# Kernel tuning notes

Hardware: AMD Instinct MI355X
Metric: run time of the kernel (lower is better)

The kernel has to match this reference:

```python
import jax, jax.numpy as jnp
import numpy as np
from jax import lax

H, P, N, G, K, CHUNK = 64, 64, 128, 1, 4, 256
D_MODEL = 2048
D_INNER = H * P            # 4096
CONV_DIM = D_INNER + 2 * G * N  # 4352
EPS = 1e-5


def setup_inputs() -> dict:
    key = jax.random.key(0)
    ks = jax.random.split(key, 6)
    s = lambda k, shape, scale: jax.random.normal(k, shape, jnp.float32) * scale
    return {
        "hidden_states": s(ks[0], (2, 2048, D_MODEL), 1.0),
        "in_proj_w": s(ks[1], (D_MODEL, D_INNER + CONV_DIM + H), D_MODEL ** -0.5),
        "conv_w": s(ks[2], (CONV_DIM, K), K ** -0.5),
        "conv_b": jnp.zeros((CONV_DIM,), jnp.float32),
        "dt_bias": jnp.ones((H,), jnp.float32),
        "A_log": jnp.log(jnp.arange(1, H + 1, dtype=jnp.float32)),
        "D_param": jnp.ones((H,), jnp.float32),
        "norm_w": jnp.ones((D_INNER,), jnp.float32),
        "out_proj_w": s(ks[3], (D_INNER, D_MODEL), D_INNER ** -0.5),
    }


def _mamba2_forward(hidden_states, in_proj_w, conv_w, conv_b, dt_bias, A_log, D_param, norm_w, out_proj_w):
    b, l, _ = hidden_states.shape
    c = l // CHUNK  # number of chunks

    # in_proj -> gate | conv channels (x,B,C) | dt
    proj = hidden_states @ in_proj_w
    gate = proj[..., :D_INNER]
    hbc = proj[..., D_INNER:D_INNER + CONV_DIM]
    dt = proj[..., D_INNER + CONV_DIM:]  # [b,l,H]

    # depthwise causal conv1d + silu
    xt = hbc.transpose(0, 2, 1)  # [b, CONV_DIM, l]
    y = lax.conv_general_dilated(
        xt, conv_w[:, None, :], window_strides=(1,), padding=[(K - 1, 0)],
        feature_group_count=CONV_DIM, dimension_numbers=("NCH", "OIH", "NCH"))
    hbc = jax.nn.silu(y + conv_b[None, :, None]).transpose(0, 2, 1)  # [b,l,CONV_DIM]

    # split into x / B / C per group (unflatten over groups as in torch code)
    per_g = D_INNER // G
    hg = hbc.reshape(b, l, G, per_g + 2 * N)
    x = hg[..., :per_g].reshape(b, l, H, P)                 # [b,l,h,p]
    Bm = hg[..., per_g:per_g + N]                            # [b,l,g,n]
    Cm = hg[..., per_g + N:]                                 # [b,l,g,n]
    hpg = H // G
    Bh = jnp.repeat(Bm, hpg, axis=2)                         # [b,l,h,n]
    Ch = jnp.repeat(Cm, hpg, axis=2)

    # dt: softplus(dt + bias), clamp per time_step_limit (0, inf)
    dt = jax.nn.softplus(dt + dt_bias)                       # [b,l,h]
    A = -jnp.exp(A_log)                                      # [h]

    # chunk the sequence
    x_c = x.reshape(b, c, CHUNK, H, P)
    B_c = Bh.reshape(b, c, CHUNK, H, N)
    C_c = Ch.reshape(b, c, CHUNK, H, N)
    dt_c = dt.reshape(b, c, CHUNK, H)

    dA = dt_c * A[None, None, None, :]                       # [b,c,L,h]
    cum = jnp.cumsum(dA, axis=2)                             # [b,c,L,h]

    # intra-chunk (diagonal block): decay[i,j] = exp(cum_i - cum_j), i>=j
    diff = cum[:, :, :, None, :] - cum[:, :, None, :, :]     # [b,c,i,j,h]
    i = jnp.arange(CHUNK)
    mask = i[:, None] >= i[None, :]
    decay = jnp.exp(jnp.where(mask[None, None, :, :, None], diff, -jnp.inf))
    scores = jnp.einsum("bcihn,bcjhn->bcijh", C_c, B_c) * decay * dt_c[:, :, None, :, :]
    Y_diag = jnp.einsum("bcijh,bcjhp->bcihp", scores, x_c)   # [b,c,L,h,p]

    # per-chunk final states
    decay_states = jnp.exp(cum[:, :, -1:, :] - cum)          # [b,c,L,h]
    states = jnp.einsum("bclh,bclhn,bclhp->bchpn", decay_states * dt_c, B_c, x_c)
    chunk_decay = jnp.exp(cum[:, :, -1, :])                  # [b,c,h]

    # inter-chunk recurrence over chunks
    def step(prev, inp):
        st, cd = inp  # [b,h,p,n], [b,h]
        new = cd[:, :, None, None] * prev + st
        return new, prev

    init = jnp.zeros((b, H, P, N), hidden_states.dtype)
    _, prev_states = lax.scan(step, init, (jnp.moveaxis(states, 1, 0), jnp.moveaxis(chunk_decay, 1, 0)))
    prev_states = jnp.moveaxis(prev_states, 0, 1)            # [b,c,h,p,n]

    state_decay_out = jnp.exp(cum)                           # [b,c,L,h]
    Y_off = jnp.einsum("bclhn,bchpn,bclh->bclhp", C_c, prev_states, state_decay_out)

    yh = (Y_diag + Y_off).reshape(b, l, H, P) + D_param[None, None, :, None] * x
    yr = yh.reshape(b, l, D_INNER)

    # gated RMSNorm
    hidden = yr * jax.nn.silu(gate)
    var = jnp.mean(hidden * hidden, axis=-1, keepdims=True)
    hidden = hidden * lax.rsqrt(var + EPS) * norm_w

    return hidden @ out_proj_w


def reference(hidden_states, in_proj_w, conv_w, conv_b, dt_bias, A_log, D_param, norm_w, out_proj_w):
    return _mamba2_forward(hidden_states, in_proj_w, conv_w, conv_b, dt_bias, A_log, D_param, norm_w, out_proj_w)
```

## Files before the change

kernel.cpp:

```cpp
#include <hip/hip_runtime.h>
#include <hip/hip_bf16.h>


typedef __attribute__((ext_vector_type(8))) _Float16 f16x8;
typedef __attribute__((ext_vector_type(4))) float f32x4;

#define GLD16(gp, lp) __builtin_amdgcn_global_load_lds( \
    (__attribute__((address_space(1))) void*)(gp),      \
    (__attribute__((address_space(3))) void*)(lp), 16, 0, 0)

__device__ __forceinline__ unsigned short f2h(float v) {
  _Float16 h = (_Float16)v;
  return *reinterpret_cast<unsigned short*>(&h);
}
__device__ __forceinline__ float h2f(unsigned short u) {
  _Float16 h = *reinterpret_cast<_Float16*>(&u);
  return (float)h;
}
__device__ __forceinline__ float siluf(float x) { return x / (1.f + expf(-x)); }

__global__ __launch_bounds__(256) void prep(const float* __restrict__ hs,
                                            const float* __restrict__ Win,
                                            _Float16* __restrict__ Ah,
                                            _Float16* __restrict__ WtH,
                                            float* __restrict__ zf) {
  __shared__ __attribute__((aligned(16))) char smemP[32768];
  const int bid = blockIdx.x;
  const int tid = threadIdx.x;
  if (bid < 1024) {
    float (*Xs)[2048] = reinterpret_cast<float (*)[2048]>(smemP);
    int t0 = bid * 4;
#pragma unroll
    for (int i = 0; i < 8; i++) {
      int e = tid * 4 + i * 1024;
      int tok = e >> 11, k = e & 2047;
      *reinterpret_cast<float4*>(&Xs[tok][k]) =
          *reinterpret_cast<const float4*>(&hs[(long)(t0 + tok) * 2048 + k]);
    }
    __syncthreads();
    int h = tid & 63, tg = tid >> 6;
    float a0 = 0.f, a1 = 0.f, a2 = 0.f, a3 = 0.f;
    const float* wcol = Win + 8448 + h;
    for (int k = 0; k < 2048; k += 4) {
      a0 = fmaf(Xs[tg][k + 0], wcol[(long)(k + 0) * 8512], a0);
      a1 = fmaf(Xs[tg][k + 1], wcol[(long)(k + 1) * 8512], a1);
      a2 = fmaf(Xs[tg][k + 2], wcol[(long)(k + 2) * 8512], a2);
      a3 = fmaf(Xs[tg][k + 3], wcol[(long)(k + 3) * 8512], a3);
    }
    zf[(long)(t0 + tg) * 64 + h] = (a0 + a1) + (a2 + a3);
  } else if (bid < 9216) {
    long i = ((long)(bid - 1024) * 256 + tid) * 4;
    float4 v = *reinterpret_cast<const float4*>(hs + i);
    ushort4 u;
    u.x = f2h(v.x); u.y = f2h(v.y); u.z = f2h(v.z); u.w = f2h(v.w);
    *reinterpret_cast<ushort4*>((unsigned short*)Ah + i) = u;
  } else {
    float (*tile)[33] = reinterpret_cast<float (*)[33]>(smemP);
    int i = bid - 9216;
    int c0 = (i % 264) * 32, r0 = (i / 264) * 32;
    int tx = tid & 31, ty = tid >> 5;
#pragma unroll
    for (int j = 0; j < 4; j++)
      tile[ty + j * 8][tx] = Win[(long)(r0 + ty + j * 8) * 8512 + c0 + tx];
    __syncthreads();
#pragma unroll
    for (int j = 0; j < 4; j++) {
      int c = c0 + ty + j * 8, r = r0 + tx;
      WtH[(long)c * 2048 + r] = (_Float16)tile[tx][ty + j * 8];
    }
  }
}

__global__ __launch_bounds__(512, 2) void gemm_in8(const _Float16* __restrict__ A,
                                                   const _Float16* __restrict__ Bt,
                                                   _Float16* __restrict__ gate,
                                                   float* __restrict__ hbcf,
                                                   float* __restrict__ rparts) {
  __shared__ __attribute__((aligned(128))) char ldsB[131072];
  const int tid = threadIdx.x;
  const int lane = tid & 63;
  const int wv = tid >> 6;
  const int wr = wv >> 2, wc = wv & 3;
  const int wg = blockIdx.x;
  const bool rem = wg >= 512;
  int by, bxn, kbase, zz;
  if (!rem) {
    const int xcd = wg & 7, j = wg >> 3;
    by = (xcd >> 2) * 8 + (j >> 3);
    bxn = (xcd & 3) * 8 + (j & 7);
    kbase = 0; zz = 0;
  } else {
    const int idx = wg - 512;
    by = idx & 15; zz = idx >> 4; bxn = 32; kbase = zz * 256;
  }

  const int srow = tid >> 3;
  const int scolg = (tid & 7) ^ (srow & 7);
  const _Float16* Ab = A + (long)by * 524288 + (long)srow * 2048 + scolg * 8 + kbase;
  const _Float16* Bb = Bt + (long)bxn * 524288 + (long)srow * 2048 + scolg * 8 + kbase;
  const int ldst = tid << 4;

#define STAGE_A(tau, h) do {                                              \
    const _Float16* g_ = Ab + (long)(h) * 262144 + (tau) * 64;            \
    char* l_ = ldsB + ((((tau) & 1) << 2) + (h)) * 16384 + ldst;          \
    GLD16(g_, l_); GLD16(g_ + 131072, l_ + 8192); } while (0)
#define STAGE_B(tau, h) do {                                              \
    const _Float16* g_ = Bb + (long)(h) * 262144 + (tau) * 64;            \
    char* l_ = ldsB + ((((tau) & 1) << 2) + 2 + (h)) * 16384 + ldst;      \
    GLD16(g_, l_); GLD16(g_ + 131072, l_ + 8192); } while (0)

  const int fr = lane & 15;
  const int c16 = (lane >> 4) ^ (fr & 7);
  const int aOff0 = wr * 16384 + fr * 128 + c16 * 16;
  const int aOff1 = aOff0 ^ 64;
  const int bOff0 = (2 + (wc >> 1)) * 16384 + ((wc & 1) * 64 + fr) * 128 + c16 * 16;
  const int bOff1 = bOff0 ^ 64;
#define RD_A(b, mi, k32) (*(const f16x8*)(ldsB + ((k32) ? aOff1 : aOff0) + (b) * 65536 + (mi) * 2048))
#define RD_B(b, ni, k32) (*(const f16x8*)(ldsB + ((k32) ? bOff1 : bOff0) + (b) * 65536 + (ni) * 2048))

#define BAR() __builtin_amdgcn_s_barrier()
#define WLG0() asm volatile("s_waitcnt lgkmcnt(0)" ::: "memory")
#define WLG8() asm volatile("s_waitcnt lgkmcnt(8)" ::: "memory")
#define WVM4() asm volatile("s_waitcnt vmcnt(4)" ::: "memory")

  f32x4 acc[8][4];
#pragma unroll
  for (int mi = 0; mi < 8; ++mi)
#pragma unroll
    for (int ni = 0; ni < 4; ++ni) acc[mi][ni] = f32x4{0.f, 0.f, 0.f, 0.f};

  STAGE_A(0, 0); STAGE_A(0, 1); STAGE_B(0, 0); STAGE_B(0, 1);
  STAGE_B(1, 0); STAGE_B(1, 1);
  WVM4(); BAR();

#define MFMA_Q(MI0, MI1, x0, x1, x2, x3, PB)                                        \
  __builtin_amdgcn_s_setprio(1);                                                    \
  _Pragma("unroll") for (int ni = 0; ni < 4; ++ni) {                                \
    acc[MI0][ni] = __builtin_amdgcn_mfma_f32_16x16x32_f16(x0, PB[ni][0], acc[MI0][ni], 0, 0, 0); \
    acc[MI0][ni] = __builtin_amdgcn_mfma_f32_16x16x32_f16(x1, PB[ni][1], acc[MI0][ni], 0, 0, 0); \
    acc[MI1][ni] = __builtin_amdgcn_mfma_f32_16x16x32_f16(x2, PB[ni][0], acc[MI1][ni], 0, 0, 0); \
    acc[MI1][ni] = __builtin_amdgcn_mfma_f32_16x16x32_f16(x3, PB[ni][1], acc[MI1][ni], 0, 0, 0); \
  }                                                                                 \
  __builtin_amdgcn_s_setprio(0);

#define ITER8(u, msk) do {                                                          \
    const int t1 = (2 * (u) + 1) & (msk);                                           \
    const int t2 = (2 * (u) + 2) & (msk);                                           \
    const int t3 = (2 * (u) + 3) & (msk);                                           \
    f16x8 PB0[4][2];                                                                \
    _Pragma("unroll") for (int ni = 0; ni < 4; ++ni) {                              \
      PB0[ni][0] = RD_B(0, ni, 0); PB0[ni][1] = RD_B(0, ni, 1); }                   \
    {                                                                               \
      f16x8 x0 = RD_A(0, 0, 0), x1 = RD_A(0, 0, 1), x2 = RD_A(0, 1, 0), x3 = RD_A(0, 1, 1); \
      STAGE_A(t1, 0); WLG8(); BAR(); WLG0();                                        \
      MFMA_Q(0, 1, x0, x1, x2, x3, PB0) BAR();                                      \
    }                                                                               \
    {                                                                               \
      f16x8 x0 = RD_A(0, 2, 0), x1 = RD_A(0, 2, 1), x2 = RD_A(0, 3, 0), x3 = RD_A(0, 3, 1); \
      STAGE_A(t1, 1); BAR(); WLG0();                                                \
      MFMA_Q(2, 3, x0, x1, x2, x3, PB0) BAR();                                      \
    }                                                                               \
    {                                                                               \
      f16x8 x0 = RD_A(0, 4, 0), x1 = RD_A(0, 4, 1), x2 = RD_A(0, 5, 0), x3 = RD_A(0, 5, 1); \
      STAGE_B(t2, 0); BAR(); WLG0();                                                \
      MFMA_Q(4, 5, x0, x1, x2, x3, PB0) BAR();                                      \
    }                                                                               \
    {                                                                               \
      f16x8 x0 = RD_A(0, 6, 0), x1 = RD_A(0, 6, 1), x2 = RD_A(0, 7, 0), x3 = RD_A(0, 7, 1); \
      STAGE_B(t2, 1); BAR(); WLG0();                                                \
      MFMA_Q(6, 7, x0, x1, x2, x3, PB0) WVM4(); BAR();                              \
    }                                                                               \
    f16x8 PB1[4][2];                                                                \
    _Pragma("unroll") for (int ni = 0; ni < 4; ++ni) {                              \
      PB1[ni][0] = RD_B(1, ni, 0); PB1[ni][1] = RD_B(1, ni, 1); }                   \
    {                                                                               \
      f16x8 x0 = RD_A(1, 0, 0), x1 = RD_A(1, 0, 1), x2 = RD_A(1, 1, 0), x3 = RD_A(1, 1, 1); \
      STAGE_A(t2, 0); WLG8(); BAR(); WLG0();                                        \
      MFMA_Q(0, 1, x0, x1, x2, x3, PB1) BAR();                                      \
    }                                                                               \
    {                                                                               \
      f16x8 x0 = RD_A(1, 2, 0), x1 = RD_A(1, 2, 1), x2 = RD_A(1, 3, 0), x3 = RD_A(1, 3, 1); \
      STAGE_A(t2, 1); BAR(); WLG0();                                                \
      MFMA_Q(2, 3, x0, x1, x2, x3, PB1) BAR();                                      \
    }                                                                               \
    {                                                                               \
      f16x8 x0 = RD_A(1, 4, 0), x1 = RD_A(1, 4, 1), x2 = RD_A(1, 5, 0), x3 = RD_A(1, 5, 1); \
      STAGE_B(t3, 0); BAR(); WLG0();                                                \
      MFMA_Q(4, 5, x0, x1, x2, x3, PB1) BAR();                                      \
    }                                                                               \
    {                                                                               \
      f16x8 x0 = RD_A(1, 6, 0), x1 = RD_A(1, 6, 1), x2 = RD_A(1, 7, 0), x3 = RD_A(1, 7, 1); \
      STAGE_B(t3, 1); BAR(); WLG0();                                                \
      MFMA_Q(6, 7, x0, x1, x2, x3, PB1) WVM4(); BAR();                              \
    }                                                                               \
  } while (0)

  if (!rem) {
    for (int u = 0; u < 16; ++u) ITER8(u, 31);
  } else {
    for (int u = 0; u < 2; ++u) ITER8(u, 3);
  }

  const int m0 = by * 256 + wr * 128;
  const int cl = lane & 15, rq = (lane >> 4) * 4;
  if (!rem) {
    const int n0 = bxn * 256 + wc * 64;
    if (bxn < 16) {
#pragma unroll
      for (int mi = 0; mi < 8; ++mi)
#pragma unroll
        for (int r = 0; r < 4; ++r) {
          long rowoff = (long)(m0 + mi * 16 + rq + r) * 4096 + n0 + cl;
#pragma unroll
          for (int ni = 0; ni < 4; ++ni) gate[rowoff + ni * 16] = (_Float16)acc[mi][ni][r];
        }
    } else {
#pragma unroll
      for (int mi = 0; mi < 8; ++mi)
#pragma unroll
        for (int r = 0; r < 4; ++r) {
          long rowoff = (long)(m0 + mi * 16 + rq + r) * 4352 + (n0 - 4096) + cl;
#pragma unroll
          for (int ni = 0; ni < 4; ++ni) hbcf[rowoff + ni * 16] = acc[mi][ni][r];
        }
    }
  } else {
    float* rp = rparts + (long)zz * 1048576;
    const int ncol = wc * 64;
#pragma unroll
    for (int mi = 0; mi < 8; ++mi)
#pragma unroll
      for (int r = 0; r < 4; ++r) {
        long rowoff = (long)(m0 + mi * 16 + rq + r) * 256 + ncol + cl;
#pragma unroll
        for (int ni = 0; ni < 4; ++ni) rp[rowoff + ni * 16] = acc[mi][ni][r];
      }
  }
#undef STAGE_A
#undef STAGE_B
#undef RD_A
#undef RD_B
#undef ITER8
}

__global__ __launch_bounds__(256) void fuse2(const float* __restrict__ zf,
                                             const float* __restrict__ dtb,
                                             const float* __restrict__ Alog,
                                             float* __restrict__ dt_f,
                                             float* __restrict__ cum_f,
                                             float* __restrict__ cuml,
                                             const float* __restrict__ rp,
                                             float* __restrict__ hbcf,
                                             const float* __restrict__ Wout,
                                             _Float16* __restrict__ WoutT) {
  __shared__ __attribute__((aligned(16))) char smem2[4352];
  const int bid = blockIdx.x;
  const int tid = threadIdx.x;
  if (bid < 16) {
    float (*segsum)[64] = reinterpret_cast<float (*)[64]>(smem2);
    int bc = bid;
    int h = tid & 63, seg = tid >> 6;
    int t0 = bc * 256;
    float Ah = -expf(Alog[h]);
    float bias = dtb[h];
    float s = 0.f;
    for (int j = 0; j < 64; j++) {
      int t = t0 + seg * 64 + j;
      float z = zf[(long)t * 64 + h] + bias;
      float v = (z > 20.f) ? z : log1pf(expf(z));
      dt_f[(long)t * 64 + h] = v;
      s += v * Ah;
    }
    segsum[seg][h] = s;
    __syncthreads();
    float run = 0.f;
    for (int k = 0; k < seg; k++) run += segsum[k][h];
    for (int j = 0; j < 64; j++) {
      int t = t0 + seg * 64 + j;
      run += dt_f[(long)t * 64 + h] * Ah;
      cum_f[(long)t * 64 + h] = run;
    }
    if (seg == 3) cuml[bc * 64 + h] = run;
  } else if (bid < 1040) {
    long e = ((long)(bid - 16) * 256 + tid) * 4;
    float4 s = *reinterpret_cast<const float4*>(rp + e);
#pragma unroll
    for (int z = 1; z < 8; ++z) {
      float4 v = *reinterpret_cast<const float4*>(rp + (long)z * 1048576 + e);
      s.x += v.x; s.y += v.y; s.z += v.z; s.w += v.w;
    }
    long row = e >> 8, col = e & 255;
    *reinterpret_cast<float4*>(hbcf + row * 4352 + 4096 + col) = s;
  } else {
    float (*tile)[33] = reinterpret_cast<float (*)[33]>(smem2);
    int i = bid - 1040;
    int c0 = (i & 63) * 32, r0 = (i >> 6) * 32;
    int tx = tid & 31, ty = tid >> 5;
#pragma unroll
    for (int j = 0; j < 4; j++)
      tile[ty + j * 8][tx] = Wout[(long)(r0 + ty + j * 8) * 2048 + c0 + tx];
    __syncthreads();
#pragma unroll
    for (int j = 0; j < 4; j++) {
      int c = c0 + ty + j * 8, r = r0 + tx;
      WoutT[(long)c * 4096 + r] = (_Float16)tile[tx][ty + j * 8];
    }
  }
}

__global__ __launch_bounds__(256) void convx(const float* __restrict__ hbcf,
                                             const float* __restrict__ convw,
                                             const float* __restrict__ convb,
                                             _Float16* __restrict__ x16,
                                             _Float16* __restrict__ B16,
                                             _Float16* __restrict__ C16,
                                             unsigned short* __restrict__ xT16) {
  __shared__ unsigned short tile[64][66];
  const int bx = blockIdx.x, t0 = blockIdx.y * 64;
  const int tid = threadIdx.x;
  const int tq = tid & 63, tg = tid >> 6;
  const int q0 = (bx < 64) ? bx * 64 : 4096 + (bx - 64) * 64;
  const int q = q0 + tq;
  const int ts = t0 + tg * 16;
  const int bstart = ts & ~2047;
  const float* colq = hbcf + q;
  float4 wq = *reinterpret_cast<const float4*>(convw + q * 4);
  float bconv = convb[q];
  float v3 = (ts - 3 >= bstart) ? colq[(long)(ts - 3) * 4352] : 0.f;
  float v2 = (ts - 2 >= bstart) ? colq[(long)(ts - 2) * 4352] : 0.f;
  float v1 = (ts - 1 >= bstart) ? colq[(long)(ts - 1) * 4352] : 0.f;
  if (bx < 64) {
#pragma unroll
    for (int j = 0; j < 16; ++j) {
      int t = ts + j;
      float v0 = colq[(long)t * 4352];
      float a = bconv + v3 * wq.x + v2 * wq.y + v1 * wq.z + v0 * wq.w;
      unsigned short o = f2h(siluf(a));
      ((unsigned short*)x16)[(long)t * 4096 + q] = o;
      tile[tg * 16 + j][tq] = o;
      v3 = v2; v2 = v1; v1 = v0;
    }
    __syncthreads();
    int tx = tid & 15, ty = tid >> 4;
#pragma unroll
    for (int i = 0; i < 4; ++i) {
      int c = ty + i * 16;
      ushort4 v;
      v.x = tile[4 * tx + 0][c]; v.y = tile[4 * tx + 1][c];
      v.z = tile[4 * tx + 2][c]; v.w = tile[4 * tx + 3][c];
      *(ushort4*)&xT16[(long)(q0 + c) * 4096 + t0 + 4 * tx] = v;
    }
  } else {
#pragma unroll
    for (int j = 0; j < 16; ++j) {
      int t = ts + j;
      float v0 = colq[(long)t * 4352];
      float a = bconv + v3 * wq.x + v2 * wq.y + v1 * wq.z + v0 * wq.w;
      _Float16 o = (_Float16)siluf(a);
      if (q < 4224) B16[(long)t * 128 + (q - 4096)] = o;
      else C16[(long)t * 128 + (q - 4224)] = o;
      v3 = v2; v2 = v1; v1 = v0;
    }
  }
}

__global__ __launch_bounds__(256) void fuse3(const unsigned short* __restrict__ xT16,
                                             const _Float16* __restrict__ B16,
                                             const _Float16* __restrict__ C16,
                                             const float* __restrict__ dt_f,
                                             const float* __restrict__ cum_f,
                                             const float* __restrict__ cuml,
                                             float* __restrict__ states,
                                             float* __restrict__ CBT,
                                             float* __restrict__ ssq) {
  __shared__ __attribute__((aligned(16))) char smem3[16384];
  const int bid = blockIdx.x;
  const int tid = threadIdx.x;
  const int wv = tid >> 6, lane = tid & 63;
  const int mr = lane & 15, koff = (lane >> 4) * 8;
  if (bid < 1024) {
    float* w_s = (float*)smem3;
    unsigned short* Aw = (unsigned short*)(smem3 + 1024);
    unsigned short* BT = (unsigned short*)(smem3 + 6144);
    int h = bid & 63, bc = bid >> 6;
    int t0 = bc * 256;
    {
      int t = t0 + tid;
      w_s[tid] = expf(cuml[bc * 64 + h] - cum_f[(long)t * 64 + h]) * dt_f[(long)t * 64 + h];
    }
    __syncthreads();
    f32x4 acc[4][2];
#pragma unroll
    for (int mi = 0; mi < 4; mi++)
#pragma unroll
      for (int nj = 0; nj < 2; nj++) acc[mi][nj] = f32x4{0.f, 0.f, 0.f, 0.f};
    for (int kt = 0; kt < 8; kt++) {
      {
        int p = tid >> 2, tq2 = tid & 3;
        const unsigned short* g = &xT16[((long)(h * 64 + p)) * 4096 + t0 + kt * 32 + tq2 * 8];
        ushort4 u0 = *(const ushort4*)g, u1 = *(const ushort4*)(g + 4);
        const float* wp = &w_s[kt * 32 + tq2 * 8];
        ushort4 o0, o1;
        o0.x = f2h(h2f(u0.x) * wp[0]); o0.y = f2h(h2f(u0.y) * wp[1]);
        o0.z = f2h(h2f(u0.z) * wp[2]); o0.w = f2h(h2f(u0.w) * wp[3]);
        o1.x = f2h(h2f(u1.x) * wp[4]); o1.y = f2h(h2f(u1.y) * wp[5]);
        o1.z = f2h(h2f(u1.z) * wp[6]); o1.w = f2h(h2f(u1.w) * wp[7]);
        *(ushort4*)&Aw[p * 40 + tq2 * 8] = o0;
        *(ushort4*)&Aw[p * 40 + tq2 * 8 + 4] = o1;
      }
      {
        int tl = tid >> 3, ng = tid & 7;
        const unsigned short* g = (const unsigned short*)B16 +
                                  ((long)(t0 + kt * 32 + tl)) * 128 + ng * 16;
#pragma unroll
        for (int j = 0; j < 16; j++) BT[(ng * 16 + j) * 40 + tl] = g[j];
      }
      __syncthreads();
      f16x8 af[4], bf[2];
#pragma unroll
      for (int mi = 0; mi < 4; mi++)
        af[mi] = *(const f16x8*)&Aw[(mi * 16 + mr) * 40 + koff];
#pragma unroll
      for (int nj = 0; nj < 2; nj++)
        bf[nj] = *(const f16x8*)&BT[((wv * 2 + nj) * 16 + mr) * 40 + koff];
#pragma unroll
      for (int mi = 0; mi < 4; mi++)
#pragma unroll
        for (int nj = 0; nj < 2; nj++)
          acc[mi][nj] = __builtin_amdgcn_mfma_f32_16x16x32_f16(af[mi], bf[nj],
                                                               acc[mi][nj], 0, 0, 0);
      __syncthreads();
    }
    int cl = lane & 15, rq = (lane >> 4) * 4;
    long base = ((long)(bc * 64 + h)) * 8192;
#pragma unroll
    for (int mi = 0; mi < 4; mi++)
#pragma unroll
      for (int r = 0; r < 4; r++) {
        int p = mi * 16 + rq + r;
#pragma unroll
        for (int nj = 0; nj < 2; nj++) {
          int n = (wv * 2 + nj) * 16 + cl;
          states[base + p * 128 + n] = acc[mi][nj][r];
        }
      }
  } else if (bid < 1088) {
    _Float16* As = (_Float16*)smem3;
    _Float16* Bs = (_Float16*)(smem3 + 8192);
    int i = bid - 1024;
    int bx = i & 1, by = (i >> 1) & 1, bz = i >> 2;
    const _Float16* Ab = B16 + (long)bz * 32768 + (long)by * 128 * 128;
    const _Float16* Bb = C16 + (long)bz * 32768 + (long)bx * 128 * 128;
    const int c0 = wv * 128 + lane;
    const int c1 = c0 + 64;
    const long ra0 = (long)(c0 >> 2) * 128 + (c0 & 3) * 8;
    const long ra1 = (long)(c1 >> 2) * 128 + (c1 & 3) * 8;
    f32x4 acc[4][4];
#pragma unroll
    for (int mi = 0; mi < 4; mi++)
#pragma unroll
      for (int ni = 0; ni < 4; ni++) acc[mi][ni] = f32x4{0.f, 0.f, 0.f, 0.f};
    const int mrow = (wv & 1) * 64 + (lane & 15);
    const int nrow = (wv >> 1) * 64 + (lane & 15);
    for (int k0 = 0; k0 < 128; k0 += 32) {
      GLD16(Ab + ra0 + k0, (char*)As + c0 * 16);
      GLD16(Ab + ra1 + k0, (char*)As + c1 * 16);
      GLD16(Bb + ra0 + k0, (char*)Bs + c0 * 16);
      GLD16(Bb + ra1 + k0, (char*)Bs + c1 * 16);
      __syncthreads();
      f16x8 af[4], bfr[4];
#pragma unroll
      for (int mi = 0; mi < 4; mi++)
        af[mi] = *(const f16x8*)(As + (mrow + mi * 16) * 32 + koff);
#pragma unroll
      for (int ni = 0; ni < 4; ni++)
        bfr[ni] = *(const f16x8*)(Bs + (nrow + ni * 16) * 32 + koff);
#pragma unroll
      for (int mi = 0; mi < 4; mi++)
#pragma unroll
        for (int ni = 0; ni < 4; ni++)
          acc[mi][ni] = __builtin_amdgcn_mfma_f32_16x16x32_f16(af[mi], bfr[ni],
                                                               acc[mi][ni], 0, 0, 0);
      __syncthreads();
    }
    const int m0 = by * 128 + (wv & 1) * 64;
    const int n0 = bx * 128 + (wv >> 1) * 64;
    const int cl = lane & 15, rq = (lane >> 4) * 4;
    const long zc = (long)bz * 65536;
#pragma unroll
    for (int mi = 0; mi < 4; mi++)
#pragma unroll
      for (int r = 0; r < 4; r++) {
        long rowoff = zc + (long)(m0 + mi * 16 + rq + r) * 256 + n0 + cl;
#pragma unroll
        for (int ni = 0; ni < 4; ni++) CBT[rowoff + ni * 16] = acc[mi][ni][r];
      }
  } else {
    int i = (bid - 1088) * 1024 + tid * 4;
    *reinterpret_cast<float4*>(&ssq[i]) = make_float4(0.f, 0.f, 0.f, 0.f);
  }
}

__global__ __launch_bounds__(256) void recur_kernel(float* __restrict__ states,
                                                    const float* __restrict__ cuml) {
  int g = blockIdx.x;
  int bh = g >> 3, js = g & 7;
  int b = bh >> 6, h = bh & 63;
  int tid = threadIdx.x;
  float4 prev = make_float4(0.f, 0.f, 0.f, 0.f);
  for (int c = 0; c < 8; c++) {
    int bc = b * 8 + c;
    float cd = expf(cuml[bc * 64 + h]);
    long o = (long)(bc * 64 + h) * 8192 + js * 1024 + tid * 4;
    float4 st = *reinterpret_cast<const float4*>(&states[o]);
    *reinterpret_cast<float4*>(&states[o]) = prev;
    prev.x = fmaf(cd, prev.x, st.x);
    prev.y = fmaf(cd, prev.y, st.y);
    prev.z = fmaf(cd, prev.z, st.z);
    prev.w = fmaf(cd, prev.w, st.w);
  }
}

__global__ __launch_bounds__(256) void yfused(const unsigned short* __restrict__ xT16,
                                              const unsigned short* __restrict__ x16,
                                              const unsigned short* __restrict__ C16,
                                              const unsigned short* __restrict__ gate,
                                              const float* __restrict__ CBTt,
                                              const float* __restrict__ states,
                                              const float* __restrict__ dt_f,
                                              const float* __restrict__ cum_f,
                                              const float* __restrict__ Dp,
                                              unsigned short* __restrict__ hid,
                                              float* __restrict__ ssq) {
  int h = blockIdx.x, bc = blockIdx.y;
  int t0 = bc * 256, tid = threadIdx.x;
  __shared__ unsigned short Sb[256 * 40];
  __shared__ unsigned short Xb[64 * 264];
  __shared__ unsigned short PS[64 * 136];
  __shared__ float c2_s[256], dt_s[256];
  int i = tid;
  c2_s[i] = cum_f[(long)(t0 + i) * 64 + h] * 1.44269504f;
  dt_s[i] = dt_f[(long)(t0 + i) * 64 + h];
  {
    int p = tid >> 2, tq = tid & 3;
    const unsigned short* g = &xT16[((long)(h * 64 + p)) * 4096 + t0 + tq * 64];
    unsigned short* l = &Xb[p * 264 + tq * 64];
#pragma unroll
    for (int c = 0; c < 8; c++)
      *(uint4*)(l + c * 8) = *(const uint4*)(g + c * 8);
  }
  {
    int p = tid >> 2, nq = tid & 3;
    const float* g = &states[((long)(bc * 64 + h)) * 8192 + p * 128 + nq * 32];
    unsigned short* l = &PS[p * 136 + nq * 32];
#pragma unroll
    for (int c = 0; c < 8; c++) {
      float4 v = *(const float4*)(g + c * 4);
      ushort4 u;
      u.x = f2h(v.x); u.y = f2h(v.y); u.z = f2h(v.z); u.w = f2h(v.w);
      *(ushort4*)(l + c * 4) = u;
    }
  }
  __syncthreads();
  float c2_i = c2_s[i];
  const float* cbcol = CBTt + (long)bc * 65536 + i;
  int wv = tid >> 6, lane = tid & 63;
  int mr = lane & 15, koff = (lane >> 4) * 8;
  f32x4 acc[4][4];
#pragma unroll
  for (int mi = 0; mi < 4; mi++)
#pragma unroll
    for (int ni = 0; ni < 4; ni++) acc[mi][ni] = f32x4{0.f, 0.f, 0.f, 0.f};
  const int ktmax = 2 * wv + 2;
  for (int kt = 0; kt < ktmax; kt++) {
    int k0 = kt * 32;
#pragma unroll
    for (int c = 0; c < 8; c++) {
      int jb = k0 + c * 4;
      float cb0 = cbcol[(long)(jb + 0) * 256];
      float cb1 = cbcol[(long)(jb + 1) * 256];
      float cb2 = cbcol[(long)(jb + 2) * 256];
      float cb3 = cbcol[(long)(jb + 3) * 256];
      ushort4 o;
      o.x = f2h((jb + 0 <= i) ? cb0 * exp2f(c2_i - c2_s[jb + 0]) * dt_s[jb + 0] : 0.f);
      o.y = f2h((jb + 1 <= i) ? cb1 * exp2f(c2_i - c2_s[jb + 1]) * dt_s[jb + 1] : 0.f);
      o.z = f2h((jb + 2 <= i) ? cb2 * exp2f(c2_i - c2_s[jb + 2]) * dt_s[jb + 2] : 0.f);
      o.w = f2h((jb + 3 <= i) ? cb3 * exp2f(c2_i - c2_s[jb + 3]) * dt_s[jb + 3] : 0.f);
      *(ushort4*)&Sb[i * 40 + c * 4] = o;
    }
    f16x8 af[4], bf[4];
#pragma unroll
    for (int mi = 0; mi < 4; mi++)
      af[mi] = *(const f16x8*)&Sb[(64 * wv + mi * 16 + mr) * 40 + koff];
#pragma unroll
    for (int ni = 0; ni < 4; ni++)
      bf[ni] = *(const f16x8*)&Xb[(ni * 16 + mr) * 264 + k0 + koff];
#pragma unroll
    for (int mi = 0; mi < 4; mi++)
#pragma unroll
      for (int ni = 0; ni < 4; ni++)
        acc[mi][ni] = __builtin_amdgcn_mfma_f32_16x16x32_f16(af[mi], bf[ni],
                                                             acc[mi][ni], 0, 0, 0);
  }
  float fac_i = exp2f(c2_i);
  for (int kn = 0; kn < 4; kn++) {
    {
      const unsigned short* g = &C16[((long)(t0 + i)) * 128 + kn * 32];
#pragma unroll
      for (int c = 0; c < 8; c++) {
        ushort4 u = *(const ushort4*)(g + c * 4);
        ushort4 o;
        o.x = f2h(h2f(u.x) * fac_i); o.y = f2h(h2f(u.y) * fac_i);
        o.z = f2h(h2f(u.z) * fac_i); o.w = f2h(h2f(u.w) * fac_i);
        *(ushort4*)&Sb[i * 40 + c * 4] = o;
      }
    }
    f16x8 af[4], bf[4];
#pragma unroll
    for (int mi = 0; mi < 4; mi++)
      af[mi] = *(const f16x8*)&Sb[(64 * wv + mi * 16 + mr) * 40 + koff];
#pragma unroll
    for (int ni = 0; ni < 4; ni++)
      bf[ni] = *(const f16x8*)&PS[(ni * 16 + mr) * 136 + kn * 32 + koff];
#pragma unroll
    for (int mi = 0; mi < 4; mi++)
#pragma unroll
      for (int ni = 0; ni < 4; ni++)
        acc[mi][ni] = __builtin_amdgcn_mfma_f32_16x16x32_f16(af[mi], bf[ni],
                                                             acc[mi][ni], 0, 0, 0);
  }
  float Dh = Dp[h];
  int cl = lane & 15, rq = (lane >> 4) * 4;
#pragma unroll
  for (int mi = 0; mi < 4; mi++)
#pragma unroll
    for (int r = 0; r < 4; r++) {
      long row = t0 + 64 * wv + mi * 16 + rq + r;
      const unsigned short* xr = &x16[row * 4096 + h * 64];
      const unsigned short* gr = &gate[row * 4096 + h * 64];
      unsigned short* hw = &hid[row * 4096 + h * 64];
      float ssp = 0.f;
#pragma unroll
      for (int ni = 0; ni < 4; ni++) {
        int p = ni * 16 + cl;
        float yv = acc[mi][ni][r] + Dh * h2f(xr[p]);
        float hv = yv * siluf(h2f(gr[p]));
        hw[p] = f2h(hv);
        ssp += hv * hv;
      }
#pragma unroll
      for (int o = 8; o > 0; o >>= 1) ssp += __shfl_down(ssp, o, 16);
      if (cl == 0) atomicAdd(&ssq[row], ssp);
    }
}

__global__ __launch_bounds__(256) void scale_kernel(const float* __restrict__ ssq,
                                                    const float* __restrict__ nw,
                                                    unsigned short* __restrict__ hid) {
  int row = blockIdx.x;
  int tid = threadIdx.x;
  float sc = rsqrtf(ssq[row] * (1.f / 4096.f) + 1e-5f);
  unsigned short* hp = hid + (long)row * 4096;
  int d0 = tid * 16;
#pragma unroll
  for (int c = 0; c < 4; c++) {
    int d = d0 + c * 4;
    ushort4 u = *reinterpret_cast<ushort4*>(&hp[d]);
    float4 w = *reinterpret_cast<const float4*>(&nw[d]);
    u.x = f2h(h2f(u.x) * sc * w.x);
    u.y = f2h(h2f(u.y) * sc * w.y);
    u.z = f2h(h2f(u.z) * sc * w.z);
    u.w = f2h(h2f(u.w) * sc * w.w);
    *reinterpret_cast<ushort4*>(&hp[d]) = u;
  }
}

__global__ __launch_bounds__(512, 2) void gemm_out8(const _Float16* __restrict__ A,
                                                    const _Float16* __restrict__ Bt,
                                                    float* __restrict__ Cp0,
                                                    float* __restrict__ Cp1) {
  __shared__ __attribute__((aligned(128))) char ldsB[131072];
  const int tid = threadIdx.x;
  const int lane = tid & 63;
  const int wv = tid >> 6;
  const int wr = wv >> 2, wc = wv & 3;
  const int wg = blockIdx.x;
  const int xcd = wg & 7, j = wg >> 3;
  const int z = j >> 4, t = j & 15;
  const int by = (xcd >> 1) * 4 + (t >> 2);
  const int bx = (xcd & 1) * 4 + (t & 3);

  const int srow = tid >> 3;
  const int scolg = (tid & 7) ^ (srow & 7);
  const _Float16* Ab = A + (long)by * 256 * 4096 + (long)z * 2048 +
                       (long)srow * 4096 + scolg * 8;
  const _Float16* Bb = Bt + (long)bx * 256 * 4096 + (long)z * 2048 +
                       (long)srow * 4096 + scolg * 8;
  const int ldst = tid << 4;

#define STAGE_A(tau, h) do {                                              \
    const _Float16* g_ = Ab + (long)(h) * 524288 + (tau) * 64;            \
    char* l_ = ldsB + ((((tau) & 1) << 2) + (h)) * 16384 + ldst;          \
    GLD16(g_, l_); GLD16(g_ + 262144, l_ + 8192); } while (0)
#define STAGE_B(tau, h) do {                                              \
    const _Float16* g_ = Bb + (long)(h) * 524288 + (tau) * 64;            \
    char* l_ = ldsB + ((((tau) & 1) << 2) + 2 + (h)) * 16384 + ldst;      \
    GLD16(g_, l_); GLD16(g_ + 262144, l_ + 8192); } while (0)

  const int fr = lane & 15;
  const int c16 = (lane >> 4) ^ (fr & 7);
  const int aOff0 = wr * 16384 + fr * 128 + c16 * 16;
  const int aOff1 = aOff0 ^ 64;
  const int bOff0 = (2 + (wc >> 1)) * 16384 + ((wc & 1) * 64 + fr) * 128 + c16 * 16;
  const int bOff1 = bOff0 ^ 64;
#define RD_A(b, mi, k32) (*(const f16x8*)(ldsB + ((k32) ? aOff1 : aOff0) + (b) * 65536 + (mi) * 2048))
#define RD_B(b, ni, k32) (*(const f16x8*)(ldsB + ((k32) ? bOff1 : bOff0) + (b) * 65536 + (ni) * 2048))

#define BAR() __builtin_amdgcn_s_barrier()
#define WLG0() asm volatile("s_waitcnt lgkmcnt(0)" ::: "memory")
#define WLG8() asm volatile("s_waitcnt lgkmcnt(8)" ::: "memory")
#define WVM4() asm volatile("s_waitcnt vmcnt(4)" ::: "memory")

  f32x4 acc[8][4];
#pragma unroll
  for (int mi = 0; mi < 8; ++mi)
#pragma unroll
    for (int ni = 0; ni < 4; ++ni) acc[mi][ni] = f32x4{0.f, 0.f, 0.f, 0.f};

  STAGE_A(0, 0); STAGE_A(0, 1); STAGE_B(0, 0); STAGE_B(0, 1);
  STAGE_B(1, 0); STAGE_B(1, 1);
  WVM4(); BAR();

#define MFMA_Q(MI0, MI1, x0, x1, x2, x3, PB)                                        \
  __builtin_amdgcn_s_setprio(1);                                                    \
  _Pragma("unroll") for (int ni = 0; ni < 4; ++ni) {                                \
    acc[MI0][ni] = __builtin_amdgcn_mfma_f32_16x16x32_f16(x0, PB[ni][0], acc[MI0][ni], 0, 0, 0); \
    acc[MI0][ni] = __builtin_amdgcn_mfma_f32_16x16x32_f16(x1, PB[ni][1], acc[MI0][ni], 0, 0, 0); \
    acc[MI1][ni] = __builtin_amdgcn_mfma_f32_16x16x32_f16(x2, PB[ni][0], acc[MI1][ni], 0, 0, 0); \
    acc[MI1][ni] = __builtin_amdgcn_mfma_f32_16x16x32_f16(x3, PB[ni][1], acc[MI1][ni], 0, 0, 0); \
  }                                                                                 \
  __builtin_amdgcn_s_setprio(0);

  for (int u = 0; u < 16; ++u) {
    const int t1 = 2 * u + 1;
    const int t2 = (2 * u + 2) & 31;
    const int t3 = (2 * u + 3) & 31;
    f16x8 PB0[4][2];
#pragma unroll
    for (int ni = 0; ni < 4; ++ni) { PB0[ni][0] = RD_B(0, ni, 0); PB0[ni][1] = RD_B(0, ni, 1); }
    {
      f16x8 x0 = RD_A(0, 0, 0), x1 = RD_A(0, 0, 1), x2 = RD_A(0, 1, 0), x3 = RD_A(0, 1, 1);
      STAGE_A(t1, 0); WLG8(); BAR(); WLG0();
      MFMA_Q(0, 1, x0, x1, x2, x3, PB0) BAR();
    }
    {
      f16x8 x0 = RD_A(0, 2, 0), x1 = RD_A(0, 2, 1), x2 = RD_A(0, 3, 0), x3 = RD_A(0, 3, 1);
      STAGE_A(t1, 1); BAR(); WLG0();
      MFMA_Q(2, 3, x0, x1, x2, x3, PB0) BAR();
    }
    {
      f16x8 x0 = RD_A(0, 4, 0), x1 = RD_A(0, 4, 1), x2 = RD_A(0, 5, 0), x3 = RD_A(0, 5, 1);
      STAGE_B(t2, 0); BAR(); WLG0();
      MFMA_Q(4, 5, x0, x1, x2, x3, PB0) BAR();
    }
    {
      f16x8 x0 = RD_A(0, 6, 0), x1 = RD_A(0, 6, 1), x2 = RD_A(0, 7, 0), x3 = RD_A(0, 7, 1);
      STAGE_B(t2, 1); BAR(); WLG0();
      MFMA_Q(6, 7, x0, x1, x2, x3, PB0) WVM4(); BAR();
    }
    f16x8 PB1[4][2];
#pragma unroll
    for (int ni = 0; ni < 4; ++ni) { PB1[ni][0] = RD_B(1, ni, 0); PB1[ni][1] = RD_B(1, ni, 1); }
    {
      f16x8 x0 = RD_A(1, 0, 0), x1 = RD_A(1, 0, 1), x2 = RD_A(1, 1, 0), x3 = RD_A(1, 1, 1);
      STAGE_A(t2, 0); WLG8(); BAR(); WLG0();
      MFMA_Q(0, 1, x0, x1, x2, x3, PB1) BAR();
    }
    {
      f16x8 x0 = RD_A(1, 2, 0), x1 = RD_A(1, 2, 1), x2 = RD_A(1, 3, 0), x3 = RD_A(1, 3, 1);
      STAGE_A(t2, 1); BAR(); WLG0();
      MFMA_Q(2, 3, x0, x1, x2, x3, PB1) BAR();
    }
    {
      f16x8 x0 = RD_A(1, 4, 0), x1 = RD_A(1, 4, 1), x2 = RD_A(1, 5, 0), x3 = RD_A(1, 5, 1);
      STAGE_B(t3, 0); BAR(); WLG0();
      MFMA_Q(4, 5, x0, x1, x2, x3, PB1) BAR();
    }
    {
      f16x8 x0 = RD_A(1, 6, 0), x1 = RD_A(1, 6, 1), x2 = RD_A(1, 7, 0), x3 = RD_A(1, 7, 1);
      STAGE_B(t3, 1); BAR(); WLG0();
      MFMA_Q(6, 7, x0, x1, x2, x3, PB1) WVM4(); BAR();
    }
  }
  const int m0 = by * 256 + wr * 128;
  const int n0 = bx * 256 + wc * 64;
  const int cl = lane & 15, rq = (lane >> 4) * 4;
  float* Cb = z ? Cp1 : Cp0;
#pragma unroll
  for (int mi = 0; mi < 8; ++mi)
#pragma unroll
    for (int r = 0; r < 4; ++r) {
      long rowoff = (long)(m0 + mi * 16 + rq + r) * 2048 + n0 + cl;
#pragma unroll
      for (int ni = 0; ni < 4; ++ni) Cb[rowoff + ni * 16] = acc[mi][ni][r];
    }
#undef STAGE_A
#undef STAGE_B
#undef RD_A
#undef RD_B
#undef BAR
#undef WLG0
#undef WLG8
#undef WVM4
#undef MFMA_Q
}

__global__ __launch_bounds__(256) void add_out(const float* __restrict__ p0,
                                               const float* __restrict__ p1,
                                               float* __restrict__ o) {
  long i = ((long)blockIdx.x * 256 + threadIdx.x) * 4;
  float4 a = *reinterpret_cast<const float4*>(p0 + i);
  float4 b = *reinterpret_cast<const float4*>(p1 + i);
  float4 r;
  r.x = a.x + b.x; r.y = a.y + b.y; r.z = a.z + b.z; r.w = a.w + b.w;
  *reinterpret_cast<float4*>(o + i) = r;
}

extern "C" void kernel_launch(void* const* d_in, const int* in_sizes, int n_in,
                              void* d_out, int out_size, void* d_ws, size_t ws_size,
                              hipStream_t stream) {
  (void)in_sizes; (void)n_in; (void)out_size; (void)ws_size;
  const float* hs    = (const float*)d_in[0];
  const float* Win   = (const float*)d_in[1];
  const float* convw = (const float*)d_in[2];
  const float* convb = (const float*)d_in[3];
  const float* dtb   = (const float*)d_in[4];
  const float* Alog  = (const float*)d_in[5];
  const float* Dp    = (const float*)d_in[6];
  const float* nw    = (const float*)d_in[7];
  const float* Wout  = (const float*)d_in[8];
  float* out = (float*)d_out;

  char* base = (char*)d_ws;
  size_t off = 0;
  auto take = [&](size_t n) { char* r = base + off; off += (n + 255) & ~(size_t)255; return r; };
  float*    hbcf  = (float*)take(4096UL * 4352 * 4);
  _Float16* gateh = (_Float16*)take(4096UL * 4096 * 2);
  _Float16* Ah    = (_Float16*)take(4096UL * 2048 * 2);
  _Float16* WtH   = (_Float16*)take(8448UL * 2048 * 2);
  _Float16* xT16  = (_Float16*)take(4096UL * 4096 * 2);
  _Float16* B16   = (_Float16*)take(4096UL * 128 * 2);
  _Float16* C16   = (_Float16*)take(4096UL * 128 * 2);
  float*    zf    = (float*)take(4096UL * 64 * 4);
  float*    dt_f  = (float*)take(4096UL * 64 * 4);
  float*    cum_f = (float*)take(4096UL * 64 * 4);
  float*    cuml  = (float*)take(16UL * 64 * 4);
  float*    ssq   = (float*)take(4096UL * 4);
  float*    CBT   = (float*)take(16UL * 256 * 256 * 4);
  float*    states= (float*)take(1024UL * 8192 * 4);
  float*    rparts = states;
  _Float16* WoutT  = Ah;
  _Float16* x16    = WtH;
  unsigned short* hid = (unsigned short*)hbcf;
  float*    oparts0 = states;
  float*    oparts1 = (float*)gateh;

  prep<<<26112, 256, 0, stream>>>(hs, Win, Ah, WtH, zf);
  gemm_in8<<<dim3(640), 512, 0, stream>>>(Ah, WtH, gateh, hbcf, rparts);
  fuse2<<<9232, 256, 0, stream>>>(zf, dtb, Alog, dt_f, cum_f, cuml,
                                  rparts, hbcf, Wout, WoutT);
  convx<<<dim3(68, 64), 256, 0, stream>>>(hbcf, convw, convb, x16, B16, C16,
                                          (unsigned short*)xT16);
  fuse3<<<1092, 256, 0, stream>>>((const unsigned short*)xT16, B16, C16,
                                  dt_f, cum_f, cuml, states, CBT, ssq);
  recur_kernel<<<1024, 256, 0, stream>>>(states, cuml);
  yfused<<<dim3(64, 16), 256, 0, stream>>>((const unsigned short*)xT16,
                                           (const unsigned short*)x16,
                                           (const unsigned short*)C16,
                                           (const unsigned short*)gateh,
                                           CBT, states, dt_f, cum_f, Dp,
                                           hid, ssq);
  scale_kernel<<<4096, 256, 0, stream>>>(ssq, nw, hid);
  gemm_out8<<<dim3(256), 512, 0, stream>>>((const _Float16*)hid, WoutT,
                                           oparts0, oparts1);
  add_out<<<8192, 256, 0, stream>>>(oparts0, oparts1, out);
}
```

Before: 701.2 us.

## Fold RMSNorm into out-proj weights and epilogue; pre-transpose B in conv

The norm weight is folded into the transposed out-projection weights, and the per-row rsqrt scale moves into the add_out epilogue, so the separate scale_kernel pass over the hidden activations is removed. The conv kernel also writes a transposed fp16 copy of B, so fuse3 loads its MFMA B fragments straight from global memory instead of doing a scalar transpose into LDS. The cost is an extra small buffer and unstaged global fragment reads. There is also a precision risk, because the fp16 hidden values going into the GEMM are now unnormalized.

```diff
diff --git a/kernel.cpp b/kernel.cpp
--- a/kernel.cpp
+++ b/kernel.cpp
@@ -252,6 +252,7 @@
                                              const float* __restrict__ rp,
                                              float* __restrict__ hbcf,
                                              const float* __restrict__ Wout,
+                                             const float* __restrict__ nw,
                                              _Float16* __restrict__ WoutT) {
   __shared__ __attribute__((aligned(16))) char smem2[4352];
   const int bid = blockIdx.x;
@@ -300,10 +301,11 @@
     for (int j = 0; j < 4; j++)
       tile[ty + j * 8][tx] = Wout[(long)(r0 + ty + j * 8) * 2048 + c0 + tx];
     __syncthreads();
+    float nwr = nw[r0 + tx];
 #pragma unroll
     for (int j = 0; j < 4; j++) {
       int c = c0 + ty + j * 8, r = r0 + tx;
-      WoutT[(long)c * 4096 + r] = (_Float16)tile[tx][ty + j * 8];
+      WoutT[(long)c * 4096 + r] = (_Float16)(tile[tx][ty + j * 8] * nwr);
     }
   }
 }
@@ -314,7 +316,8 @@
                                              _Float16* __restrict__ x16,
                                              _Float16* __restrict__ B16,
                                              _Float16* __restrict__ C16,
-                                             unsigned short* __restrict__ xT16) {
+                                             unsigned short* __restrict__ xT16,
+                                             unsigned short* __restrict__ BT16) {
   __shared__ unsigned short tile[64][66];
   const int bx = blockIdx.x, t0 = blockIdx.y * 64;
   const int tid = threadIdx.x;
@@ -350,6 +353,28 @@
       v.z = tile[4 * tx + 2][c]; v.w = tile[4 * tx + 3][c];
       *(ushort4*)&xT16[(long)(q0 + c) * 4096 + t0 + 4 * tx] = v;
     }
+  } else if (bx < 66) {
+    const int n0 = q0 - 4096;
+#pragma unroll
+    for (int j = 0; j < 16; ++j) {
+      int t = ts + j;
+      float v0 = colq[(long)t * 4352];
+      float a = bconv + v3 * wq.x + v2 * wq.y + v1 * wq.z + v0 * wq.w;
+      unsigned short o = f2h(siluf(a));
+      ((unsigned short*)B16)[(long)t * 128 + (q - 4096)] = o;
+      tile[tg * 16 + j][tq] = o;
+      v3 = v2; v2 = v1; v1 = v0;
+    }
+    __syncthreads();
+    int tx = tid & 15, ty = tid >> 4;
+#pragma unroll
+    for (int i = 0; i < 4; ++i) {
+      int c = ty + i * 16;
+      ushort4 v;
+      v.x = tile[4 * tx + 0][c]; v.y = tile[4 * tx + 1][c];
+      v.z = tile[4 * tx + 2][c]; v.w = tile[4 * tx + 3][c];
+      *(ushort4*)&BT16[(long)(n0 + c) * 4096 + t0 + 4 * tx] = v;
+    }
   } else {
 #pragma unroll
     for (int j = 0; j < 16; ++j) {
@@ -357,14 +382,14 @@
       float v0 = colq[(long)t * 4352];
       float a = bconv + v3 * wq.x + v2 * wq.y + v1 * wq.z + v0 * wq.w;
       _Float16 o = (_Float16)siluf(a);
-      if (q < 4224) B16[(long)t * 128 + (q - 4096)] = o;
-      else C16[(long)t * 128 + (q - 4224)] = o;
+      C16[(long)t * 128 + (q - 4224)] = o;
       v3 = v2; v2 = v1; v1 = v0;
     }
   }
 }
 
 __global__ __launch_bounds__(256) void fuse3(const unsigned short* __restrict__ xT16,
+                                             const unsigned short* __restrict__ BT16,
                                              const _Float16* __restrict__ B16,
                                              const _Float16* __restrict__ C16,
                                              const float* __restrict__ dt_f,
@@ -381,7 +406,6 @@
   if (bid < 1024) {
     float* w_s = (float*)smem3;
     unsigned short* Aw = (unsigned short*)(smem3 + 1024);
-    unsigned short* BT = (unsigned short*)(smem3 + 6144);
     int h = bid & 63, bc = bid >> 6;
     int t0 = bc * 256;
     {
@@ -394,6 +418,7 @@
     for (int mi = 0; mi < 4; mi++)
 #pragma unroll
       for (int nj = 0; nj < 2; nj++) acc[mi][nj] = f32x4{0.f, 0.f, 0.f, 0.f};
+    const unsigned short* btb = BT16 + t0 + koff;
     for (int kt = 0; kt < 8; kt++) {
       {
         int p = tid >> 2, tq2 = tid & 3;
@@ -408,13 +433,6 @@
         *(ushort4*)&Aw[p * 40 + tq2 * 8] = o0;
         *(ushort4*)&Aw[p * 40 + tq2 * 8 + 4] = o1;
       }
-      {
-        int tl = tid >> 3, ng = tid & 7;
-        const unsigned short* g = (const unsigned short*)B16 +
-                                  ((long)(t0 + kt * 32 + tl)) * 128 + ng * 16;
-#pragma unroll
-        for (int j = 0; j < 16; j++) BT[(ng * 16 + j) * 40 + tl] = g[j];
-      }
       __syncthreads();
       f16x8 af[4], bf[2];
 #pragma unroll
@@ -422,7 +440,7 @@
         af[mi] = *(const f16x8*)&Aw[(mi * 16 + mr) * 40 + koff];
 #pragma unroll
       for (int nj = 0; nj < 2; nj++)
-        bf[nj] = *(const f16x8*)&BT[((wv * 2 + nj) * 16 + mr) * 40 + koff];
+        bf[nj] = *(const f16x8*)(btb + (long)((wv * 2 + nj) * 16 + mr) * 4096 + kt * 32);
 #pragma unroll
       for (int mi = 0; mi < 4; mi++)
 #pragma unroll
@@ -654,27 +672,6 @@
     }
 }
 
-__global__ __launch_bounds__(256) void scale_kernel(const float* __restrict__ ssq,
-                                                    const float* __restrict__ nw,
-                                                    unsigned short* __restrict__ hid) {
-  int row = blockIdx.x;
-  int tid = threadIdx.x;
-  float sc = rsqrtf(ssq[row] * (1.f / 4096.f) + 1e-5f);
-  unsigned short* hp = hid + (long)row * 4096;
-  int d0 = tid * 16;
-#pragma unroll
-  for (int c = 0; c < 4; c++) {
-    int d = d0 + c * 4;
-    ushort4 u = *reinterpret_cast<ushort4*>(&hp[d]);
-    float4 w = *reinterpret_cast<const float4*>(&nw[d]);
-    u.x = f2h(h2f(u.x) * sc * w.x);
-    u.y = f2h(h2f(u.y) * sc * w.y);
-    u.z = f2h(h2f(u.z) * sc * w.z);
-    u.w = f2h(h2f(u.w) * sc * w.w);
-    *reinterpret_cast<ushort4*>(&hp[d]) = u;
-  }
-}
-
 __global__ __launch_bounds__(512, 2) void gemm_out8(const _Float16* __restrict__ A,
                                                     const _Float16* __restrict__ Bt,
                                                     float* __restrict__ Cp0,
@@ -817,12 +814,15 @@
 
 __global__ __launch_bounds__(256) void add_out(const float* __restrict__ p0,
                                                const float* __restrict__ p1,
+                                               const float* __restrict__ ssq,
                                                float* __restrict__ o) {
   long i = ((long)blockIdx.x * 256 + threadIdx.x) * 4;
+  float sc = rsqrtf(ssq[i >> 11] * (1.f / 4096.f) + 1e-5f);
   float4 a = *reinterpret_cast<const float4*>(p0 + i);
   float4 b = *reinterpret_cast<const float4*>(p1 + i);
   float4 r;
-  r.x = a.x + b.x; r.y = a.y + b.y; r.z = a.z + b.z; r.w = a.w + b.w;
+  r.x = (a.x + b.x) * sc; r.y = (a.y + b.y) * sc;
+  r.z = (a.z + b.z) * sc; r.w = (a.w + b.w) * sc;
   *reinterpret_cast<float4*>(o + i) = r;
 }
 
@@ -850,6 +850,7 @@
   _Float16* WtH   = (_Float16*)take(8448UL * 2048 * 2);
   _Float16* xT16  = (_Float16*)take(4096UL * 4096 * 2);
   _Float16* B16   = (_Float16*)take(4096UL * 128 * 2);
+  _Float16* BT16  = (_Float16*)take(128UL * 4096 * 2);
   _Float16* C16   = (_Float16*)take(4096UL * 128 * 2);
   float*    zf    = (float*)take(4096UL * 64 * 4);
   float*    dt_f  = (float*)take(4096UL * 64 * 4);
@@ -868,10 +869,12 @@
   prep<<<26112, 256, 0, stream>>>(hs, Win, Ah, WtH, zf);
   gemm_in8<<<dim3(640), 512, 0, stream>>>(Ah, WtH, gateh, hbcf, rparts);
   fuse2<<<9232, 256, 0, stream>>>(zf, dtb, Alog, dt_f, cum_f, cuml,
-                                  rparts, hbcf, Wout, WoutT);
+                                  rparts, hbcf, Wout, nw, WoutT);
   convx<<<dim3(68, 64), 256, 0, stream>>>(hbcf, convw, convb, x16, B16, C16,
-                                          (unsigned short*)xT16);
-  fuse3<<<1092, 256, 0, stream>>>((const unsigned short*)xT16, B16, C16,
+                                          (unsigned short*)xT16,
+                                          (unsigned short*)BT16);
+  fuse3<<<1092, 256, 0, stream>>>((const unsigned short*)xT16,
+                                  (const unsigned short*)BT16, B16, C16,
                                   dt_f, cum_f, cuml, states, CBT, ssq);
   recur_kernel<<<1024, 256, 0, stream>>>(states, cuml);
   yfused<<<dim3(64, 16), 256, 0, stream>>>((const unsigned short*)xT16,
@@ -880,8 +883,7 @@
                                            (const unsigned short*)gateh,
                                            CBT, states, dt_f, cum_f, Dp,
                                            hid, ssq);
-  scale_kernel<<<4096, 256, 0, stream>>>(ssq, nw, hid);
   gemm_out8<<<dim3(256), 512, 0, stream>>>((const _Float16*)hid, WoutT,
                                            oparts0, oparts1);
-  add_out<<<8192, 256, 0, stream>>>(oparts0, oparts1, out);
-}
+  add_out<<<8192, 256, 0, stream>>>(oparts0, oparts1, ssq, out);
+}
```

Result: no change. 695.8 us (-0.8%).
